# Optimization experiments

Measured on AMD Instinct MI355X. Metric: run time of the kernel, lower is better.

Reference implementation:

```python
import jax, jax.numpy as jnp
import numpy as np

N = 1_000_000          # number of query points
POINT_DIMS = 2         # (x, y) coordinates
NUM_EMB = 6572         # number of video frames
EMB_DIM = 32
HIDDEN = 128


def setup_inputs() -> dict:
    key = jax.random.key(0)
    ks = jax.random.split(key, 10)
    x = jax.random.uniform(ks[0], (N, POINT_DIMS), dtype=jnp.float32)
    # fractional frame index in [0, NUM_EMB - 1)
    embeddings = jax.random.uniform(ks[1], (N,), dtype=jnp.float32) * (NUM_EMB - 1)
    em_table = jax.random.normal(ks[2], (NUM_EMB, EMB_DIM), dtype=jnp.float32) * 0.1
    in0 = POINT_DIMS + EMB_DIM
    W0 = jax.random.normal(ks[3], (in0, HIDDEN), dtype=jnp.float32) / np.sqrt(in0)
    b0 = jax.random.normal(ks[4], (HIDDEN,), dtype=jnp.float32) * 0.01
    W1 = jax.random.normal(ks[5], (HIDDEN, HIDDEN), dtype=jnp.float32) / np.sqrt(HIDDEN)
    b1 = jax.random.normal(ks[6], (HIDDEN,), dtype=jnp.float32) * 0.01
    W2 = jax.random.normal(ks[7], (HIDDEN, 1), dtype=jnp.float32) / np.sqrt(HIDDEN)
    b2 = jax.random.normal(ks[8], (1,), dtype=jnp.float32) * 0.01
    return {"x": x, "embeddings": embeddings, "em_table": em_table,
            "W0": W0, "b0": b0, "W1": W1, "b1": b1, "W2": W2, "b2": b2}


def reference(x, embeddings, em_table, W0, b0, W1, b1, W2, b2):
    num_emb = em_table.shape[0]
    em1 = embeddings.astype(jnp.int32)                       # floor (inputs >= 0)
    em2 = jnp.minimum(em1 + 1, num_emb - 1)                  # clamp(em1+1, max=E-1)
    res = (embeddings - em1.astype(jnp.float32))[:, None]    # [N, 1]
    e1 = em_table[em1]                                       # [N, 32] gather
    e2 = em_table[em2]                                       # [N, 32] gather
    em = e1 + (e2 - e1) * res                                # lerp
    h = jnp.concatenate((x, em), axis=1) @ W0 + b0           # [N, 128]
    h = jnp.clip(h, 0.0, 1.0)
    h = jnp.clip(h @ W1 + b1, 0.0, 1.0)
    out = jax.nn.sigmoid(h @ W2 + b2)                        # [N, 1]
    return out
```

## Files before the change

### kernel.cpp

```cpp
#include <hip/hip_runtime.h>
#include <hip/hip_bf16.h>


using bf16x8 = __attribute__((ext_vector_type(8))) short;
using f32x4  = __attribute__((ext_vector_type(4))) float;

#define NPTS    1000000
#define NUMEMB  6572
#define HID     128
#define M_IT    64
#define A0S     72
#define H0S     136
#define TILES   (NPTS / M_IT)
#define NBLOCKS 768

__device__ __forceinline__ unsigned short bf16r(float f) {
    unsigned u;
    __builtin_memcpy(&u, &f, 4);
    u = (u + 0x7fffu + ((u >> 16) & 1u)) >> 16;
    return (unsigned short)u;
}
__device__ __forceinline__ unsigned pk2(float a, float b) {
    float2 f2; f2.x = a; f2.y = b;
    __hip_bfloat162 h = __float22bfloat162_rn(f2);
    unsigned u;
    __builtin_memcpy(&u, &h, 4);
    return u;
}
__device__ __forceinline__ float clamp01(float x) {
    return __builtin_amdgcn_fmed3f(x, 0.f, 1.f);
}

__global__ __launch_bounds__(256, 3)
void mlp_fused(const float* __restrict__ x,
               const float* __restrict__ emb,
               const float* __restrict__ em_table,
               const float* __restrict__ W0, const float* __restrict__ b0,
               const float* __restrict__ W1, const float* __restrict__ b1,
               const float* __restrict__ W2, const float* __restrict__ b2,
               float* __restrict__ out)
{
    __shared__ __align__(16) unsigned short A0[M_IT * A0S];
    __shared__ __align__(16) unsigned short H0[M_IT * H0S];
    __shared__ __align__(16) float PART[16][M_IT];

    const int tid  = threadIdx.x;
    const int lane = tid & 63;
    const int nq   = tid >> 6;
    const int q    = lane >> 4;
    const int cl   = lane & 15;

    for (int i = tid; i < M_IT * A0S; i += 256) A0[i] = 0;

    bf16x8 w0t[2][2];
    for (int hb = 0; hb < 2; ++hb)
        for (int kt = 0; kt < 2; ++kt) {
            const int col = nq * 32 + hb * 16 + cl;
            bf16x8 v;
            #pragma unroll
            for (int e = 0; e < 8; ++e) {
                const int k = kt * 32 + q * 8 + e;
                float val = 0.f;
                if (k < 32)       val = W0[(2 + k) * HID + col];
                else if (k == 32) val = W0[0 * HID + col];
                else if (k == 33) val = W0[1 * HID + col];
                v[e] = (short)bf16r(val);
            }
            w0t[hb][kt] = v;
        }

    bf16x8 w1t[2][4];
    for (int hb = 0; hb < 2; ++hb)
        for (int kt = 0; kt < 4; ++kt) {
            const int col = nq * 32 + hb * 16 + cl;
            bf16x8 v;
            #pragma unroll
            for (int e = 0; e < 8; ++e) {
                const int k = kt * 32 + q * 8 + e;
                v[e] = (short)bf16r(W1[k * HID + col]);
            }
            w1t[hb][kt] = v;
        }

    f32x4 b0q[2], b1q[2], w2q[2];
    for (int hb = 0; hb < 2; ++hb)
        for (int r = 0; r < 4; ++r) {
            const int h = nq * 32 + hb * 16 + q * 4 + r;
            b0q[hb][r] = b0[h];
            b1q[hb][r] = b1[h];
            w2q[hb][r] = W2[h];
        }
    const float bias2 = b2[0];

    __syncthreads();

    for (int t = blockIdx.x; t < TILES; t += gridDim.x) {
        const int base = t * M_IT;

        {
            const int p  = tid >> 2;
            const int s  = tid & 3;
            const int gp = base + p;
            const float fe = emb[gp];
            const int e1 = (int)fe;
            int e2 = e1 + 1; if (e2 > NUMEMB - 1) e2 = NUMEMB - 1;
            const float r = fe - (float)e1;
            const float4* p1 = (const float4*)(em_table + e1 * 32 + s * 8);
            const float4* p2 = (const float4*)(em_table + e2 * 32 + s * 8);
            const float4 a0v = p1[0], a1v = p1[1];
            const float4 c0v = p2[0], c1v = p2[1];
            uint4 d;
            d.x = pk2(a0v.x + (c0v.x - a0v.x) * r, a0v.y + (c0v.y - a0v.y) * r);
            d.y = pk2(a0v.z + (c0v.z - a0v.z) * r, a0v.w + (c0v.w - a0v.w) * r);
            d.z = pk2(a1v.x + (c1v.x - a1v.x) * r, a1v.y + (c1v.y - a1v.y) * r);
            d.w = pk2(a1v.z + (c1v.z - a1v.z) * r, a1v.w + (c1v.w - a1v.w) * r);
            *(uint4*)&A0[p * A0S + s * 8] = d;
            if (s == 0) {
                const float2 xv = *(const float2*)(x + 2 * gp);
                *(unsigned*)&A0[p * A0S + 32] = pk2(xv.x, xv.y);
            }
        }
        __syncthreads();

        f32x4 acc[4][2];
        #pragma unroll
        for (int pb = 0; pb < 4; ++pb)
            #pragma unroll
            for (int hb = 0; hb < 2; ++hb)
                acc[pb][hb] = b0q[hb];
        #pragma unroll
        for (int pb = 0; pb < 4; ++pb) {
            #pragma unroll
            for (int kt = 0; kt < 2; ++kt) {
                bf16x8 bfrag = *(const bf16x8*)
                    &A0[(pb * 16 + cl) * A0S + kt * 32 + q * 8];
                #pragma unroll
                for (int hb = 0; hb < 2; ++hb)
                    acc[pb][hb] = __builtin_amdgcn_mfma_f32_16x16x32_bf16(
                        w0t[hb][kt], bfrag, acc[pb][hb], 0, 0, 0);
            }
        }
        #pragma unroll
        for (int pb = 0; pb < 4; ++pb)
            #pragma unroll
            for (int hb = 0; hb < 2; ++hb) {
                const f32x4 v = acc[pb][hb];
                uint2 dd;
                dd.x = pk2(clamp01(v[0]), clamp01(v[1]));
                dd.y = pk2(clamp01(v[2]), clamp01(v[3]));
                *(uint2*)&H0[(pb * 16 + cl) * H0S
                             + nq * 32 + hb * 16 + q * 4] = dd;
            }
        __syncthreads();

        #pragma unroll
        for (int pb = 0; pb < 4; ++pb)
            #pragma unroll
            for (int hb = 0; hb < 2; ++hb)
                acc[pb][hb] = b1q[hb];
        #pragma unroll
        for (int pb = 0; pb < 4; ++pb) {
            #pragma unroll
            for (int kt = 0; kt < 4; ++kt) {
                bf16x8 bfrag = *(const bf16x8*)
                    &H0[(pb * 16 + cl) * H0S + kt * 32 + q * 8];
                #pragma unroll
                for (int hb = 0; hb < 2; ++hb)
                    acc[pb][hb] = __builtin_amdgcn_mfma_f32_16x16x32_bf16(
                        w1t[hb][kt], bfrag, acc[pb][hb], 0, 0, 0);
            }
        }

        #pragma unroll
        for (int pb = 0; pb < 4; ++pb) {
            float s = 0.f;
            #pragma unroll
            for (int hb = 0; hb < 2; ++hb) {
                const f32x4 v = acc[pb][hb];
                s += clamp01(v[0]) * w2q[hb][0];
                s += clamp01(v[1]) * w2q[hb][1];
                s += clamp01(v[2]) * w2q[hb][2];
                s += clamp01(v[3]) * w2q[hb][3];
            }
            PART[nq * 4 + q][pb * 16 + cl] = s;
        }
        __syncthreads();

        if (tid < 64) {
            float z = bias2;
            #pragma unroll
            for (int i = 0; i < 16; ++i) z += PART[i][tid];
            out[base + tid] = 1.f / (1.f + __expf(-z));
        }
    }
}

extern "C" void kernel_launch(void* const* d_in, const int* in_sizes, int n_in,
                              void* d_out, int out_size, void* d_ws, size_t ws_size,
                              hipStream_t stream) {
    const float* x   = (const float*)d_in[0];
    const float* emb = (const float*)d_in[1];
    const float* emt = (const float*)d_in[2];
    const float* W0  = (const float*)d_in[3];
    const float* b0  = (const float*)d_in[4];
    const float* W1  = (const float*)d_in[5];
    const float* b1  = (const float*)d_in[6];
    const float* W2  = (const float*)d_in[7];
    const float* b2  = (const float*)d_in[8];
    mlp_fused<<<NBLOCKS, 256, 0, stream>>>(x, emb, emt, W0, b0, W1, b1, W2, b2,
                                           (float*)d_out);
}
```

Before: 133.2 us.

## Software-pipeline embedding gathers across tiles and reuse own H0 fragment from registers

Adds a two-deep register prefetch pipeline: the emb/x values for tile t+2 and the em_table gather rows for tile t+1 are loaded during the current tile's compute, so global gather latency overlaps the MFMA work. It also remaps the hidden-column permutation of W0/W1/bias so that each wave's layer-0 output matches the layer-1 B-fragment layout, which lets the wave use its own slice from registers instead of reading it back from LDS and store it as a single 16-byte write. The cost is higher register pressure at launch_bounds(256,3), which could cause spills or lower occupancy.

```diff
diff --git a/kernel.cpp b/kernel.cpp
--- a/kernel.cpp
+++ b/kernel.cpp
@@ -49,13 +49,16 @@
     const int nq   = tid >> 6;
     const int q    = lane >> 4;
     const int cl   = lane & 15;
+    const int p    = tid >> 2;
+    const int s    = tid & 3;
 
     for (int i = tid; i < M_IT * A0S; i += 256) A0[i] = 0;
 
+    const int hcol = nq * 32 + (cl >> 2) * 8 + (cl & 3);
     bf16x8 w0t[2][2];
     for (int hb = 0; hb < 2; ++hb)
         for (int kt = 0; kt < 2; ++kt) {
-            const int col = nq * 32 + hb * 16 + cl;
+            const int col = hcol + hb * 4;
             bf16x8 v;
             #pragma unroll
             for (int e = 0; e < 8; ++e) {
@@ -72,7 +75,7 @@
     bf16x8 w1t[2][4];
     for (int hb = 0; hb < 2; ++hb)
         for (int kt = 0; kt < 4; ++kt) {
-            const int col = nq * 32 + hb * 16 + cl;
+            const int col = hcol + hb * 4;
             bf16x8 v;
             #pragma unroll
             for (int e = 0; e < 8; ++e) {
@@ -85,40 +88,48 @@
     f32x4 b0q[2], b1q[2], w2q[2];
     for (int hb = 0; hb < 2; ++hb)
         for (int r = 0; r < 4; ++r) {
-            const int h = nq * 32 + hb * 16 + q * 4 + r;
+            const int h = nq * 32 + q * 8 + hb * 4 + r;
             b0q[hb][r] = b0[h];
             b1q[hb][r] = b1[h];
             w2q[hb][r] = W2[h];
         }
     const float bias2 = b2[0];
 
+    int t = blockIdx.x;
+    float  feA, feB;
+    float2 xvA = {0.f, 0.f}, xvB = {0.f, 0.f};
+    float4 gA0, gA1, gA2, gA3;
+    {
+        const int gp = t * M_IT + p;
+        feA = emb[gp];
+        if (s == 0) xvA = *(const float2*)(x + 2 * gp);
+        const int e1 = (int)feA;
+        const int e2 = (e1 + 1 < NUMEMB) ? e1 + 1 : NUMEMB - 1;
+        const float4* p1 = (const float4*)(em_table + e1 * 32 + s * 8);
+        const float4* p2 = (const float4*)(em_table + e2 * 32 + s * 8);
+        gA0 = p1[0]; gA1 = p1[1]; gA2 = p2[0]; gA3 = p2[1];
+    }
+    {
+        int t1 = t + gridDim.x; if (t1 >= TILES) t1 = t;
+        const int gp = t1 * M_IT + p;
+        feB = emb[gp];
+        if (s == 0) xvB = *(const float2*)(x + 2 * gp);
+    }
+
     __syncthreads();
 
-    for (int t = blockIdx.x; t < TILES; t += gridDim.x) {
+    for (; t < TILES; t += gridDim.x) {
         const int base = t * M_IT;
 
         {
-            const int p  = tid >> 2;
-            const int s  = tid & 3;
-            const int gp = base + p;
-            const float fe = emb[gp];
-            const int e1 = (int)fe;
-            int e2 = e1 + 1; if (e2 > NUMEMB - 1) e2 = NUMEMB - 1;
-            const float r = fe - (float)e1;
-            const float4* p1 = (const float4*)(em_table + e1 * 32 + s * 8);
-            const float4* p2 = (const float4*)(em_table + e2 * 32 + s * 8);
-            const float4 a0v = p1[0], a1v = p1[1];
-            const float4 c0v = p2[0], c1v = p2[1];
+            const float r = feA - (float)(int)feA;
             uint4 d;
-            d.x = pk2(a0v.x + (c0v.x - a0v.x) * r, a0v.y + (c0v.y - a0v.y) * r);
-            d.y = pk2(a0v.z + (c0v.z - a0v.z) * r, a0v.w + (c0v.w - a0v.w) * r);
-            d.z = pk2(a1v.x + (c1v.x - a1v.x) * r, a1v.y + (c1v.y - a1v.y) * r);
-            d.w = pk2(a1v.z + (c1v.z - a1v.z) * r, a1v.w + (c1v.w - a1v.w) * r);
+            d.x = pk2(gA0.x + (gA2.x - gA0.x) * r, gA0.y + (gA2.y - gA0.y) * r);
+            d.y = pk2(gA0.z + (gA2.z - gA0.z) * r, gA0.w + (gA2.w - gA0.w) * r);
+            d.z = pk2(gA1.x + (gA3.x - gA1.x) * r, gA1.y + (gA3.y - gA1.y) * r);
+            d.w = pk2(gA1.z + (gA3.z - gA1.z) * r, gA1.w + (gA3.w - gA1.w) * r);
             *(uint4*)&A0[p * A0S + s * 8] = d;
-            if (s == 0) {
-                const float2 xv = *(const float2*)(x + 2 * gp);
-                *(unsigned*)&A0[p * A0S + 32] = pk2(xv.x, xv.y);
-            }
+            if (s == 0) *(unsigned*)&A0[p * A0S + 32] = pk2(xvA.x, xvA.y);
         }
         __syncthreads();
 
@@ -140,17 +151,18 @@
                         w0t[hb][kt], bfrag, acc[pb][hb], 0, 0, 0);
             }
         }
-        #pragma unroll
-        for (int pb = 0; pb < 4; ++pb)
-            #pragma unroll
-            for (int hb = 0; hb < 2; ++hb) {
-                const f32x4 v = acc[pb][hb];
-                uint2 dd;
-                dd.x = pk2(clamp01(v[0]), clamp01(v[1]));
-                dd.y = pk2(clamp01(v[2]), clamp01(v[3]));
-                *(uint2*)&H0[(pb * 16 + cl) * H0S
-                             + nq * 32 + hb * 16 + q * 4] = dd;
-            }
+        uint4 own[4];
+        #pragma unroll
+        for (int pb = 0; pb < 4; ++pb) {
+            const f32x4 v0 = acc[pb][0], v1 = acc[pb][1];
+            uint4 w;
+            w.x = pk2(clamp01(v0[0]), clamp01(v0[1]));
+            w.y = pk2(clamp01(v0[2]), clamp01(v0[3]));
+            w.z = pk2(clamp01(v1[0]), clamp01(v1[1]));
+            w.w = pk2(clamp01(v1[2]), clamp01(v1[3]));
+            own[pb] = w;
+            *(uint4*)&H0[(pb * 16 + cl) * H0S + nq * 32 + q * 8] = w;
+        }
         __syncthreads();
 
         #pragma unroll
@@ -162,8 +174,13 @@
         for (int pb = 0; pb < 4; ++pb) {
             #pragma unroll
             for (int kt = 0; kt < 4; ++kt) {
-                bf16x8 bfrag = *(const bf16x8*)
-                    &H0[(pb * 16 + cl) * H0S + kt * 32 + q * 8];
+                bf16x8 bfrag;
+                if (kt == nq) {
+                    __builtin_memcpy(&bfrag, &own[pb], 16);
+                } else {
+                    bfrag = *(const bf16x8*)
+                        &H0[(pb * 16 + cl) * H0S + kt * 32 + q * 8];
+                }
                 #pragma unroll
                 for (int hb = 0; hb < 2; ++hb)
                     acc[pb][hb] = __builtin_amdgcn_mfma_f32_16x16x32_bf16(
@@ -171,18 +188,34 @@
             }
         }
 
-        #pragma unroll
-        for (int pb = 0; pb < 4; ++pb) {
-            float s = 0.f;
+        float4 nB0, nB1, nB2, nB3;
+        {
+            const int e1 = (int)feB;
+            const int e2 = (e1 + 1 < NUMEMB) ? e1 + 1 : NUMEMB - 1;
+            const float4* p1 = (const float4*)(em_table + e1 * 32 + s * 8);
+            const float4* p2 = (const float4*)(em_table + e2 * 32 + s * 8);
+            nB0 = p1[0]; nB1 = p1[1]; nB2 = p2[0]; nB3 = p2[1];
+        }
+        float feC; float2 xvC = {0.f, 0.f};
+        {
+            int t2 = t + 2 * (int)gridDim.x; if (t2 >= TILES) t2 = t;
+            const int gp = t2 * M_IT + p;
+            feC = emb[gp];
+            if (s == 0) xvC = *(const float2*)(x + 2 * gp);
+        }
+
+        #pragma unroll
+        for (int pb = 0; pb < 4; ++pb) {
+            float sum = 0.f;
             #pragma unroll
             for (int hb = 0; hb < 2; ++hb) {
                 const f32x4 v = acc[pb][hb];
-                s += clamp01(v[0]) * w2q[hb][0];
-                s += clamp01(v[1]) * w2q[hb][1];
-                s += clamp01(v[2]) * w2q[hb][2];
-                s += clamp01(v[3]) * w2q[hb][3];
-            }
-            PART[nq * 4 + q][pb * 16 + cl] = s;
+                sum += clamp01(v[0]) * w2q[hb][0];
+                sum += clamp01(v[1]) * w2q[hb][1];
+                sum += clamp01(v[2]) * w2q[hb][2];
+                sum += clamp01(v[3]) * w2q[hb][3];
+            }
+            PART[nq * 4 + q][pb * 16 + cl] = sum;
         }
         __syncthreads();
 
@@ -192,6 +225,9 @@
             for (int i = 0; i < 16; ++i) z += PART[i][tid];
             out[base + tid] = 1.f / (1.f + __expf(-z));
         }
+
+        feA = feB; xvA = xvB; gA0 = nB0; gA1 = nB1; gA2 = nB2; gA3 = nB3;
+        feB = feC; xvB = xvC;
     }
 }
 
```

Result: slower. 185.1 us (+39.0%).
